# Optimization experiments

Measured on AMD Instinct MI355X. Metric: run time of the kernel, lower is better.

Reference implementation:

```python
import jax, jax.numpy as jnp
import numpy as np


def setup_inputs() -> dict:
    key = jax.random.key(0)
    k1, k2 = jax.random.split(key)
    B, T, K, D = 8, 4096, 1024, 256
    x = jax.random.normal(k1, (B, T, D), dtype=jnp.float32)
    codebook = jax.random.normal(k2, (K, D), dtype=jnp.float32)
    return {"x": x, "codebook": codebook}


def reference(x, codebook):
    # Faithful to: dist = tf.norm(z_e - lookup_, axis=-1); argmin(dist, -1).
    # argmin of the Euclidean norm == argmin of the squared distance, so we
    # instead of materializing the (B, T, k, d) broadcast intermediate.
    x2 = jnp.sum(x * x, axis=-1, keepdims=True)          # (B, T, 1)
    c2 = jnp.sum(codebook * codebook, axis=-1)           # (k,)
    xc = jnp.einsum('btd,kd->btk', x, codebook)          # (B, T, k)
    dist2 = x2 + c2 - 2.0 * xc                           # (B, T, k)
    return jnp.argmin(dist2, axis=-1)                    # (B, T) int
```

## Files before the change

kernel.cpp:

```cpp
#include <hip/hip_runtime.h>
#include <stdint.h>

typedef __attribute__((ext_vector_type(8))) _Float16 f16x8;
typedef __attribute__((ext_vector_type(4))) float f32x4;

#define MARG 0.09375f

__device__ __forceinline__ void glds16(const void* g, void* l) {
  __builtin_amdgcn_global_load_lds(
      (const __attribute__((address_space(1))) void*)g,
      (__attribute__((address_space(3))) void*)l, 16, 0, 0);
}

__device__ __forceinline__ unsigned short f2h(float f) {
  return __builtin_bit_cast(unsigned short, (_Float16)f);
}

__global__ __launch_bounds__(256) void vq_prep_x(const float* __restrict__ x,
                                                 unsigned short* __restrict__ xh,
                                                 int* __restrict__ count) {
  size_t base = ((size_t)blockIdx.x * 256 + threadIdx.x) * 16;
#pragma unroll
  for (int q = 0; q < 4; ++q) {
    float4 v = *reinterpret_cast<const float4*>(x + base + q * 4);
    ushort4 h;
    h.x = f2h(v.x); h.y = f2h(v.y); h.z = f2h(v.z); h.w = f2h(v.w);
    *reinterpret_cast<ushort4*>(xh + base + q * 4) = h;
  }
  if (blockIdx.x == 0 && threadIdx.x == 0) *count = 0;
}

__global__ __launch_bounds__(256) void vq_prep_cb(const float* __restrict__ cb,
                                                  unsigned short* __restrict__ cbh,
                                                  float* __restrict__ hc) {
  int w = threadIdx.x >> 6, lane = threadIdx.x & 63;
  int row = blockIdx.x * 4 + w;
  size_t off = (size_t)row * 256 + lane * 4;
  float4 v = *reinterpret_cast<const float4*>(cb + off);
  ushort4 h;
  h.x = f2h(v.x); h.y = f2h(v.y); h.z = f2h(v.z); h.w = f2h(v.w);
  *reinterpret_cast<ushort4*>(cbh + off) = h;
  float s = v.x * v.x + v.y * v.y + v.z * v.z + v.w * v.w;
#pragma unroll
  for (int m = 32; m >= 1; m >>= 1) s += __shfl_xor(s, m, 64);
  if (lane == 0) hc[row] = 0.5f * s;
}

__global__ __launch_bounds__(512, 4) void vq_mfma_kernel(
    const unsigned short* __restrict__ xh, const unsigned short* __restrict__ cbh,
    const float* __restrict__ hc, int* __restrict__ out,
    int* __restrict__ list, int* __restrict__ count) {
  __shared__ unsigned short sm[20480];
  __shared__ float c2s[1024];
  __shared__ float cbv[4][64];
  __shared__ int   cbi[4][64];
  __shared__ float csv[4][64];

  const int tid = threadIdx.x;
  const int lane = tid & 63;
  const int wave = tid >> 6;
  const int wr = wave >> 2;
  const int wc = wave & 3;
  const int l15 = lane & 15;
  const int l4  = lane >> 4;
  const int bswz = (blockIdx.x & 7) * 64 + (blockIdx.x >> 3);
  const int r0 = bswz * 64;

  reinterpret_cast<float2*>(c2s)[tid] = reinterpret_cast<const float2*>(hc)[tid];

  const int sA   = tid & 255;
  const int srow = sA >> 2;
  const int schA = (sA & 3) ^ ((sA >> 3) & 3);

  auto stage = [&](int T1) {
    const int p = T1 & 1;
    const int n0 = (T1 >> 3) << 8;
    const int d0 = (T1 & 7) << 5;
    unsigned short* A = sm + p * 2048;
    unsigned short* B = sm + 4096 + p * 8192;
    glds16(xh + (size_t)(r0 + srow) * 256 + d0 + schA * 8, A + sA * 8);
#pragma unroll
    for (int r = 0; r < 2; ++r) {
      int idx = r * 512 + tid;
      int bch = (idx & 3) ^ ((idx >> 3) & 3);
      glds16(cbh + (size_t)(n0 + (idx >> 2)) * 256 + d0 + bch * 8, B + idx * 8);
    }
  };

  float bestv[2][4], secondv[2][4];
  int besti[2][4];
#pragma unroll
  for (int tr = 0; tr < 2; ++tr)
#pragma unroll
    for (int g = 0; g < 4; ++g) {
      bestv[tr][g] = -3.4e38f; secondv[tr][g] = -3.4e38f; besti[tr][g] = 0;
    }

  stage(0);

  const int swzf = (l15 >> 1) & 3;

  int T = 0;
  for (int nt = 0; nt < 4; ++nt) {
    f32x4 acc[2][4];
#pragma unroll
    for (int tr = 0; tr < 2; ++tr)
#pragma unroll
      for (int tc = 0; tc < 4; ++tc) acc[tr][tc] = (f32x4){0.f, 0.f, 0.f, 0.f};

    for (int dt = 0; dt < 8; ++dt, ++T) {
      const int p = T & 1;
      if (T < 31) {
        stage(T + 1);
        asm volatile("s_waitcnt vmcnt(3)" ::: "memory");
      } else {
        asm volatile("s_waitcnt vmcnt(0)" ::: "memory");
      }
      __builtin_amdgcn_s_barrier();

      const unsigned short* A = sm + p * 2048;
      const unsigned short* B = sm + 4096 + p * 8192;

      f16x8 af[2], bf[4];
#pragma unroll
      for (int tr = 0; tr < 2; ++tr) {
        int arow = wr * 32 + tr * 16 + l15;
        af[tr] = *reinterpret_cast<const f16x8*>(A + arow * 32 + (l4 ^ swzf) * 8);
      }
#pragma unroll
      for (int tc = 0; tc < 4; ++tc) {
        int bcol = wc * 64 + tc * 16 + l15;
        bf[tc] = *reinterpret_cast<const f16x8*>(B + bcol * 32 + (l4 ^ swzf) * 8);
      }

#pragma unroll
      for (int tr = 0; tr < 2; ++tr)
#pragma unroll
        for (int tc = 0; tc < 4; ++tc)
          acc[tr][tc] = __builtin_amdgcn_mfma_f32_16x16x32_f16(af[tr], bf[tc], acc[tr][tc], 0, 0, 0);

      asm volatile("s_waitcnt lgkmcnt(0)" ::: "memory");
      __builtin_amdgcn_s_barrier();
    }

    const int cb0 = nt * 256 + wc * 64 + l15;
    float hcv[4];
#pragma unroll
    for (int tc = 0; tc < 4; ++tc) hcv[tc] = c2s[cb0 + tc * 16];
#pragma unroll
    for (int tr = 0; tr < 2; ++tr)
#pragma unroll
      for (int tc = 0; tc < 4; ++tc) {
        const int code = cb0 + tc * 16;
#pragma unroll
        for (int g = 0; g < 4; ++g) {
          float s = acc[tr][tc][g] - hcv[tc];
          bool gt = s > bestv[tr][g];
          float ns = gt ? bestv[tr][g] : fmaxf(secondv[tr][g], s);
          bestv[tr][g] = gt ? s : bestv[tr][g];
          besti[tr][g] = gt ? code : besti[tr][g];
          secondv[tr][g] = ns;
        }
      }
  }

#pragma unroll
  for (int tr = 0; tr < 2; ++tr)
#pragma unroll
    for (int g = 0; g < 4; ++g) {
      float bv = bestv[tr][g]; int bi = besti[tr][g]; float sv = secondv[tr][g];
#pragma unroll
      for (int m = 1; m < 16; m <<= 1) {
        float ov = __shfl_xor(bv, m, 64);
        int   oi = __shfl_xor(bi, m, 64);
        float os = __shfl_xor(sv, m, 64);
        sv = fmaxf(fmaxf(sv, os), fminf(bv, ov));
        bool gt = (ov > bv) || (ov == bv && oi < bi);
        bv = gt ? ov : bv;
        bi = gt ? oi : bi;
      }
      if (l15 == 0) {
        int rl = wr * 32 + tr * 16 + l4 * 4 + g;
        cbv[wc][rl] = bv; cbi[wc][rl] = bi; csv[wc][rl] = sv;
      }
    }

  __syncthreads();
  if (tid < 64) {
    float bv = cbv[0][tid]; int bi = cbi[0][tid]; float sv = csv[0][tid];
#pragma unroll
    for (int w2 = 1; w2 < 4; ++w2) {
      float ov = cbv[w2][tid]; int oi = cbi[w2][tid]; float os = csv[w2][tid];
      sv = fmaxf(fmaxf(sv, os), fminf(bv, ov));
      bool gt = (ov > bv) || (ov == bv && oi < bi);
      bv = gt ? ov : bv;
      bi = gt ? oi : bi;
    }
    out[r0 + tid] = bi;
    if (sv >= bv - MARG) {
      int slot = atomicAdd(count, 1);
      list[slot] = r0 + tid;
    }
  }
}

__global__ __launch_bounds__(512) void vq_cleanup(const float* __restrict__ x,
                                                  const float* __restrict__ cb,
                                                  const float* __restrict__ hc,
                                                  const int* __restrict__ list,
                                                  const int* __restrict__ count,
                                                  int* __restrict__ out) {
  __shared__ float xt[4][256];
  __shared__ int rowids[4];
  __shared__ float wbv[8][4];
  __shared__ int   wbi[8][4];
  const int tid = threadIdx.x;
  const int wave = tid >> 6;
  const int n = *count;

  for (int t0 = blockIdx.x * 4; t0 < n; t0 += gridDim.x * 4) {
    __syncthreads();
    if (tid < 4) rowids[tid] = (t0 + tid < n) ? list[t0 + tid] : -1;
    __syncthreads();
    {
      int j = tid >> 7, seg = tid & 127;
      int row = rowids[j];
      if (row < 0) row = rowids[0];
      *reinterpret_cast<float2*>(&xt[j][seg * 2]) =
          *reinterpret_cast<const float2*>(x + (size_t)row * 256 + seg * 2);
    }
    __syncthreads();

    float acc0[4], acc1[4];
#pragma unroll
    for (int j = 0; j < 4; ++j) { acc0[j] = 0.f; acc1[j] = 0.f; }

    const float* c0 = cb + (size_t)tid * 256;
    const float* c1 = cb + (size_t)(512 + tid) * 256;
#pragma unroll 4
    for (int d0 = 0; d0 < 256; d0 += 4) {
      float4 ca = *reinterpret_cast<const float4*>(c0 + d0);
      float4 cd = *reinterpret_cast<const float4*>(c1 + d0);
#pragma unroll
      for (int j = 0; j < 4; ++j) {
        float4 xv = *reinterpret_cast<const float4*>(&xt[j][d0]);
        acc0[j] = fmaf(ca.x, xv.x, acc0[j]);
        acc0[j] = fmaf(ca.y, xv.y, acc0[j]);
        acc0[j] = fmaf(ca.z, xv.z, acc0[j]);
        acc0[j] = fmaf(ca.w, xv.w, acc0[j]);
        acc1[j] = fmaf(cd.x, xv.x, acc1[j]);
        acc1[j] = fmaf(cd.y, xv.y, acc1[j]);
        acc1[j] = fmaf(cd.z, xv.z, acc1[j]);
        acc1[j] = fmaf(cd.w, xv.w, acc1[j]);
      }
    }

    const float h0 = hc[tid];
    const float h1 = hc[512 + tid];

#pragma unroll
    for (int j = 0; j < 4; ++j) {
      float bv = acc0[j] - h0; int bi = tid;
      float s1 = acc1[j] - h1;
      if (s1 > bv) { bv = s1; bi = 512 + tid; }
#pragma unroll
      for (int m = 1; m < 64; m <<= 1) {
        float ov = __shfl_xor(bv, m, 64);
        int   oi = __shfl_xor(bi, m, 64);
        bool gt = (ov > bv) || (ov == bv && oi < bi);
        bv = gt ? ov : bv;
        bi = gt ? oi : bi;
      }
      if ((tid & 63) == 0) { wbv[wave][j] = bv; wbi[wave][j] = bi; }
    }
    __syncthreads();
    if (tid < 4 && rowids[tid] >= 0) {
      float bv = wbv[0][tid]; int bi = wbi[0][tid];
#pragma unroll
      for (int w2 = 1; w2 < 8; ++w2) {
        float ov = wbv[w2][tid]; int oi = wbi[w2][tid];
        if (ov > bv || (ov == bv && oi < bi)) { bv = ov; bi = oi; }
      }
      out[rowids[tid]] = bi;
    }
  }
}

#define BM 128
#define BN 256
#define BD 32
#define NT 512

__global__ __launch_bounds__(256) void vq_c2_kernel(const float* __restrict__ cb,
                                                    float* __restrict__ halfc2) {
  int row  = blockIdx.x * 4 + (threadIdx.x >> 6);
  int lane = threadIdx.x & 63;
  float4 v = *reinterpret_cast<const float4*>(cb + (size_t)row * 256 + lane * 4);
  float s = v.x * v.x + v.y * v.y + v.z * v.z + v.w * v.w;
#pragma unroll
  for (int m = 32; m >= 1; m >>= 1) s += __shfl_xor(s, m, 64);
  if (lane == 0) halfc2[row] = 0.5f * s;
}

__global__ __launch_bounds__(NT, 2) void vq_argmin_kernel(
    const float* __restrict__ x, const float* __restrict__ cb,
    const float* __restrict__ halfc2, int* __restrict__ out) {
  __shared__ float lds[2][(BM + BN) * BD];
  __shared__ float c2s[1024];
  const int tid = threadIdx.x;
  const int w   = tid >> 6;
  const int tc  = tid & 31;
  const int tr  = tid >> 5;
  const int r0  = blockIdx.x * BM;
  reinterpret_cast<float2*>(c2s)[tid] = reinterpret_cast<const float2*>(halfc2)[tid];
  const int sA  = tr & 7;
  const int sB  = tc & 7;
  const int sAB = sA ^ sB;
  const int cho = (((tid & 7) ^ w)) * 4;
  const int sub = tid >> 3;
  float bestv[8]; int besti[8];
#pragma unroll
  for (int i = 0; i < 8; ++i) { bestv[i] = -3.4e38f; besti[i] = 0; }
  auto stage = [&](int n0, int d0, int p) {
    float* dst  = &lds[p][0];
    float* dstB = dst + BM * BD;
#pragma unroll
    for (int r = 0; r < 2; ++r) {
      int t2 = r * NT + tid;
      glds16(x + (size_t)(r0 + r * 64 + sub) * 256 + d0 + cho, dst + t2 * 4);
    }
#pragma unroll
    for (int r = 0; r < 4; ++r) {
      int t2 = r * NT + tid;
      glds16(cb + (size_t)(n0 + r * 64 + sub) * 256 + d0 + cho, dstB + t2 * 4);
    }
  };
  stage(0, 0, 0);
  int t = 0;
  for (int nt = 0; nt < 4; ++nt) {
    float acc[8][8];
#pragma unroll
    for (int i = 0; i < 8; ++i)
#pragma unroll
      for (int j = 0; j < 8; ++j) acc[i][j] = 0.f;
    for (int dt = 0; dt < 8; ++dt, ++t) {
      const int p = t & 1;
      if (t < 31) {
        const int t1 = t + 1;
        stage((t1 >> 3) * BN, (t1 & 7) * BD, t1 & 1);
        asm volatile("s_waitcnt vmcnt(6)" ::: "memory");
      } else {
        asm volatile("s_waitcnt vmcnt(0)" ::: "memory");
      }
      __builtin_amdgcn_s_barrier();
      const float* pA = &lds[p][tr * 8 * BD];
      const float* pB = &lds[p][BM * BD + tc * 8 * BD];
#pragma unroll
      for (int cc = 0; cc < 8; ++cc) {
        const float* pBc = pB + ((cc ^ sAB) << 2);
        float4 a[8], b[8];
#pragma unroll
        for (int i = 0; i < 8; ++i)
          a[i] = *reinterpret_cast<const float4*>(pA + i * BD + cc * 4);
#pragma unroll
        for (int j = 0; j < 8; ++j)
          b[j] = *reinterpret_cast<const float4*>(pBc + j * BD);
#pragma unroll
        for (int i = 0; i < 8; ++i)
#pragma unroll
          for (int j = 0; j < 8; ++j) {
            acc[i][j] = fmaf(a[i].x, b[j].x, acc[i][j]);
            acc[i][j] = fmaf(a[i].y, b[j].y, acc[i][j]);
            acc[i][j] = fmaf(a[i].z, b[j].z, acc[i][j]);
            acc[i][j] = fmaf(a[i].w, b[j].w, acc[i][j]);
          }
      }
      asm volatile("s_waitcnt lgkmcnt(0)" ::: "memory");
      __builtin_amdgcn_s_barrier();
    }
    const int n0 = nt * BN;
#pragma unroll
    for (int j = 0; j < 8; ++j) {
      const int code = n0 + tc * 8 + j;
      const float hc = c2s[code];
#pragma unroll
      for (int i = 0; i < 8; ++i) {
        float s = acc[i][j] - hc;
        if (s > bestv[i]) { bestv[i] = s; besti[i] = code; }
      }
    }
  }
#pragma unroll
  for (int i = 0; i < 8; ++i) {
#pragma unroll
    for (int m = 1; m <= 16; m <<= 1) {
      float ov = __shfl_xor(bestv[i], m, 64);
      int   oi = __shfl_xor(besti[i], m, 64);
      if (ov > bestv[i] || (ov == bestv[i] && oi < besti[i])) { bestv[i] = ov; besti[i] = oi; }
    }
  }
  if (tc == 0) {
#pragma unroll
    for (int i = 0; i < 8; ++i) out[r0 + tr * 8 + i] = besti[i];
  }
}

extern "C" void kernel_launch(void* const* d_in, const int* in_sizes, int n_in,
                              void* d_out, int out_size, void* d_ws, size_t ws_size,
                              hipStream_t stream) {
  const float* x  = (const float*)d_in[0];
  const float* cb = (const float*)d_in[1];
  int* out = (int*)d_out;

  const size_t OFF_XH = 0;
  const size_t OFF_CH = OFF_XH + (size_t)32768 * 256 * 2;
  const size_t OFF_HC = OFF_CH + (size_t)1024 * 256 * 2;
  const size_t OFF_LS = OFF_HC + (size_t)1024 * 4;
  const size_t OFF_CT = OFF_LS + (size_t)32768 * 4;
  const size_t NEED   = OFF_CT + 64;

  if (ws_size >= NEED) {
    unsigned short* xh  = (unsigned short*)((char*)d_ws + OFF_XH);
    unsigned short* cbh = (unsigned short*)((char*)d_ws + OFF_CH);
    float* hc  = (float*)((char*)d_ws + OFF_HC);
    int* list  = (int*)((char*)d_ws + OFF_LS);
    int* count = (int*)((char*)d_ws + OFF_CT);

    hipLaunchKernelGGL(vq_prep_x, dim3(2048), dim3(256), 0, stream, x, xh, count);
    hipLaunchKernelGGL(vq_prep_cb, dim3(256), dim3(256), 0, stream, cb, cbh, hc);
    hipLaunchKernelGGL(vq_mfma_kernel, dim3(512), dim3(512), 0, stream,
                       xh, cbh, hc, out, list, count);
    hipLaunchKernelGGL(vq_cleanup, dim3(512), dim3(512), 0, stream,
                       x, cb, hc, list, count, out);
  } else {
    float* c2 = (float*)d_ws;
    hipLaunchKernelGGL(vq_c2_kernel, dim3(256), dim3(256), 0, stream, cb, c2);
    hipLaunchKernelGGL(vq_argmin_kernel, dim3(32768 / BM), dim3(NT), 0, stream,
                       x, cb, c2, out);
  }
}
```

Baseline: 83.96 us.

## Fuse x fp16 conversion into MFMA kernel with resident swizzled A tile in LDS

Removes the separate x-to-fp16 prep kernel. Each block now loads its 64 rows of fp32 x directly, converts them to fp16 and keeps the whole 64x256 A tile resident in an XOR-swizzled LDS buffer for all codebook tiles, so only B is streamed per step. The count reset moves into the codebook prep kernel. This drops a kernel launch and the round trip through the fp16 x buffer in global memory, at the cost of more LDS per block (possible occupancy loss) and a non-pipelined fp32 load at kernel start.

```diff
diff --git a/kernel.cpp b/kernel.cpp
--- a/kernel.cpp
+++ b/kernel.cpp
@@ -16,23 +16,10 @@
   return __builtin_bit_cast(unsigned short, (_Float16)f);
 }
 
-__global__ __launch_bounds__(256) void vq_prep_x(const float* __restrict__ x,
-                                                 unsigned short* __restrict__ xh,
-                                                 int* __restrict__ count) {
-  size_t base = ((size_t)blockIdx.x * 256 + threadIdx.x) * 16;
-#pragma unroll
-  for (int q = 0; q < 4; ++q) {
-    float4 v = *reinterpret_cast<const float4*>(x + base + q * 4);
-    ushort4 h;
-    h.x = f2h(v.x); h.y = f2h(v.y); h.z = f2h(v.z); h.w = f2h(v.w);
-    *reinterpret_cast<ushort4*>(xh + base + q * 4) = h;
-  }
-  if (blockIdx.x == 0 && threadIdx.x == 0) *count = 0;
-}
-
 __global__ __launch_bounds__(256) void vq_prep_cb(const float* __restrict__ cb,
                                                   unsigned short* __restrict__ cbh,
-                                                  float* __restrict__ hc) {
+                                                  float* __restrict__ hc,
+                                                  int* __restrict__ count) {
   int w = threadIdx.x >> 6, lane = threadIdx.x & 63;
   int row = blockIdx.x * 4 + w;
   size_t off = (size_t)row * 256 + lane * 4;
@@ -44,13 +31,15 @@
 #pragma unroll
   for (int m = 32; m >= 1; m >>= 1) s += __shfl_xor(s, m, 64);
   if (lane == 0) hc[row] = 0.5f * s;
+  if (blockIdx.x == 0 && threadIdx.x == 0) *count = 0;
 }
 
 __global__ __launch_bounds__(512, 4) void vq_mfma_kernel(
-    const unsigned short* __restrict__ xh, const unsigned short* __restrict__ cbh,
+    const float* __restrict__ x, const unsigned short* __restrict__ cbh,
     const float* __restrict__ hc, int* __restrict__ out,
     int* __restrict__ list, int* __restrict__ count) {
-  __shared__ unsigned short sm[20480];
+  __shared__ unsigned short Alds[16384];
+  __shared__ unsigned short Blds[16384];
   __shared__ float c2s[1024];
   __shared__ float cbv[4][64];
   __shared__ int   cbi[4][64];
@@ -68,17 +57,30 @@
 
   reinterpret_cast<float2*>(c2s)[tid] = reinterpret_cast<const float2*>(hc)[tid];
 
-  const int sA   = tid & 255;
-  const int srow = sA >> 2;
-  const int schA = (sA & 3) ^ ((sA >> 3) & 3);
+  {
+    const int row = tid >> 3;
+    const int cc  = tid & 7;
+    const float* src = x + (size_t)(r0 + row) * 256 + cc * 32;
+    unsigned short hv[32];
+#pragma unroll
+    for (int q = 0; q < 8; ++q) {
+      float4 v = *reinterpret_cast<const float4*>(src + q * 4);
+      hv[q * 4 + 0] = f2h(v.x); hv[q * 4 + 1] = f2h(v.y);
+      hv[q * 4 + 2] = f2h(v.z); hv[q * 4 + 3] = f2h(v.w);
+    }
+    char* base = reinterpret_cast<char*>(Alds);
+#pragma unroll
+    for (int g = 0; g < 4; ++g) {
+      int byte = (row * 512 + cc * 64 + g * 16) ^ ((row & 7) << 4);
+      *reinterpret_cast<f16x8*>(base + byte) = *reinterpret_cast<const f16x8*>(&hv[g * 8]);
+    }
+  }
 
   auto stage = [&](int T1) {
     const int p = T1 & 1;
     const int n0 = (T1 >> 3) << 8;
     const int d0 = (T1 & 7) << 5;
-    unsigned short* A = sm + p * 2048;
-    unsigned short* B = sm + 4096 + p * 8192;
-    glds16(xh + (size_t)(r0 + srow) * 256 + d0 + schA * 8, A + sA * 8);
+    unsigned short* B = Blds + p * 8192;
 #pragma unroll
     for (int r = 0; r < 2; ++r) {
       int idx = r * 512 + tid;
@@ -96,9 +98,16 @@
       bestv[tr][g] = -3.4e38f; secondv[tr][g] = -3.4e38f; besti[tr][g] = 0;
     }
 
+  __syncthreads();
   stage(0);
 
   const int swzf = (l15 >> 1) & 3;
+  int abase[2];
+#pragma unroll
+  for (int tr = 0; tr < 2; ++tr) {
+    int arow = wr * 32 + tr * 16 + l15;
+    abase[tr] = (arow * 512 + l4 * 16) ^ ((arow & 7) << 4);
+  }
 
   int T = 0;
   for (int nt = 0; nt < 4; ++nt) {
@@ -112,21 +121,19 @@
       const int p = T & 1;
       if (T < 31) {
         stage(T + 1);
-        asm volatile("s_waitcnt vmcnt(3)" ::: "memory");
+        asm volatile("s_waitcnt vmcnt(2)" ::: "memory");
       } else {
         asm volatile("s_waitcnt vmcnt(0)" ::: "memory");
       }
       __builtin_amdgcn_s_barrier();
 
-      const unsigned short* A = sm + p * 2048;
-      const unsigned short* B = sm + 4096 + p * 8192;
+      const char* Ab = reinterpret_cast<const char*>(Alds);
+      const unsigned short* B = Blds + p * 8192;
 
       f16x8 af[2], bf[4];
 #pragma unroll
-      for (int tr = 0; tr < 2; ++tr) {
-        int arow = wr * 32 + tr * 16 + l15;
-        af[tr] = *reinterpret_cast<const f16x8*>(A + arow * 32 + (l4 ^ swzf) * 8);
-      }
+      for (int tr = 0; tr < 2; ++tr)
+        af[tr] = *reinterpret_cast<const f16x8*>(Ab + (abase[tr] ^ (dt * 64)));
 #pragma unroll
       for (int tc = 0; tc < 4; ++tc) {
         int bcol = wc * 64 + tc * 16 + l15;
@@ -412,24 +419,21 @@
   const float* cb = (const float*)d_in[1];
   int* out = (int*)d_out;
 
-  const size_t OFF_XH = 0;
-  const size_t OFF_CH = OFF_XH + (size_t)32768 * 256 * 2;
+  const size_t OFF_CH = 0;
   const size_t OFF_HC = OFF_CH + (size_t)1024 * 256 * 2;
   const size_t OFF_LS = OFF_HC + (size_t)1024 * 4;
   const size_t OFF_CT = OFF_LS + (size_t)32768 * 4;
   const size_t NEED   = OFF_CT + 64;
 
   if (ws_size >= NEED) {
-    unsigned short* xh  = (unsigned short*)((char*)d_ws + OFF_XH);
     unsigned short* cbh = (unsigned short*)((char*)d_ws + OFF_CH);
     float* hc  = (float*)((char*)d_ws + OFF_HC);
     int* list  = (int*)((char*)d_ws + OFF_LS);
     int* count = (int*)((char*)d_ws + OFF_CT);
 
-    hipLaunchKernelGGL(vq_prep_x, dim3(2048), dim3(256), 0, stream, x, xh, count);
-    hipLaunchKernelGGL(vq_prep_cb, dim3(256), dim3(256), 0, stream, cb, cbh, hc);
+    hipLaunchKernelGGL(vq_prep_cb, dim3(256), dim3(256), 0, stream, cb, cbh, hc, count);
     hipLaunchKernelGGL(vq_mfma_kernel, dim3(512), dim3(512), 0, stream,
-                       xh, cbh, hc, out, list, count);
+                       x, cbh, hc, out, list, count);
     hipLaunchKernelGGL(vq_cleanup, dim3(512), dim3(512), 0, stream,
                        x, cb, hc, list, count, out);
   } else {
```

New measurement: 75.87 us. 9.6% less time.
